# Kernel tuning notes

Measured on AMD Instinct MI355X. Metric: run time of the kernel, lower is better.

The kernel has to match this reference:

```python
import jax, jax.numpy as jnp
import numpy as np

B, C, N = 8, 512, 2048
C8 = C // 8


def setup_inputs() -> dict:
    key = jax.random.key(0)
    kx, kq, kk, kv, kg = jax.random.split(key, 5)
    return {
        "x": jax.random.normal(kx, (B, C, N), dtype=jnp.float32),
        "Wq": jax.random.normal(kq, (C8, C), dtype=jnp.float32) * (1.0 / np.sqrt(C)),
        "Wk": jax.random.normal(kk, (C8, C), dtype=jnp.float32) * (1.0 / np.sqrt(C)),
        "Wv": jax.random.normal(kv, (C, C), dtype=jnp.float32) * (1.0 / np.sqrt(C)),
        # torch init is gamma=0.0; use a small random value so the attention
        # branch contributes to the output.
        "gamma": jax.random.uniform(kg, (1,), dtype=jnp.float32),
    }


def reference(x, Wq, Wk, Wv, gamma):
    # 1x1 convs == per-position linear maps over channels
    f = jnp.einsum("oc,bcn->bon", Wq, x)   # [B, C/8, N]
    g = jnp.einsum("oc,bcn->bon", Wk, x)   # [B, C/8, N]
    h = jnp.einsum("oc,bcn->bon", Wv, x)   # [B, C,   N]
    # scores[b,n,m] = sum_c f[b,c,n] * g[b,c,m]  (unscaled, as in source)
    scores = jnp.einsum("bcn,bcm->bnm", f, g)  # [B, N, N]
    # softmax over dim=1 (the query-position axis) — atypical but faithful
    beta = jax.nn.softmax(scores, axis=1)
    # o = gamma * h @ beta + x
    o = gamma[0] * jnp.einsum("bcn,bnm->bcm", h, beta) + x
    return o
```

## Files before the change

kernel.cpp:

```cpp
#include <hip/hip_runtime.h>
#include <hip/hip_bf16.h>
#include <math.h>

#define NB 8
#define NC 512
#define NN 2048

typedef unsigned short u16;
typedef __attribute__((ext_vector_type(8))) short short8;
typedef __attribute__((ext_vector_type(4))) float f32x4;

__device__ __forceinline__ float bf16_to_f32(u16 v) {
  union { unsigned int u; float f; } c; c.u = ((unsigned int)v) << 16; return c.f;
}
__device__ __forceinline__ u16 f32_to_bf16(float f) {
  __hip_bfloat16 h = __float2bfloat16(f);
  union { __hip_bfloat16 h; u16 u; } c; c.h = h; return c.u;
}
__device__ __forceinline__ void split2(float v, unsigned short& hi, unsigned short& lo) {
  hi = f32_to_bf16(v);
  lo = f32_to_bf16(v - bf16_to_f32(hi));
}

__device__ __forceinline__ void stage128x32(const u16* __restrict__ src, size_t row_base,
                                            int selems, int k0, u16* lds, int tid) {
#pragma unroll
  for (int s = 0; s < 2; ++s) {
    int flat = s * 4096 + tid * 16;
    int row = flat >> 6;
    int kb  = flat & 63;
    const char* g = (const char*)(src + (row_base + row) * (size_t)selems + k0) + kb;
    u16* l = lds + s * 2048 + (tid & ~63) * 8;
    __builtin_amdgcn_global_load_lds(
        (const __attribute__((address_space(1))) unsigned int*)g,
        (__attribute__((address_space(3))) unsigned int*)l, 16, 0, 0);
  }
}

__device__ __forceinline__ void stage128x64_sw(const u16* __restrict__ src, size_t row_base,
                                               int selems, int k0, u16* lds, int tid) {
#pragma unroll
  for (int s = 0; s < 4; ++s) {
    int flat = s * 4096 + tid * 16;
    int row   = flat >> 7;
    int chunk = (flat >> 4) & 7;
    int kb    = (chunk ^ (row & 7)) << 4;
    const char* g = (const char*)(src + (row_base + row) * (size_t)selems + k0) + kb;
    u16* l = lds + s * 2048 + (tid & ~63) * 8;
    __builtin_amdgcn_global_load_lds(
        (const __attribute__((address_space(1))) unsigned int*)g,
        (__attribute__((address_space(3))) unsigned int*)l, 16, 0, 0);
  }
}

__global__ __launch_bounds__(256)
void wsplit_kernel(const float* __restrict__ Wq, const float* __restrict__ Wk,
                   const float* __restrict__ Wv, u16* __restrict__ Whi,
                   u16* __restrict__ Wlo) {
  int idx = (blockIdx.x * 256 + threadIdx.x) * 4;
  int r = idx >> 9, c = idx & 511;
  const float* src;
  if (r < 64)       src = Wq + (size_t)r * NC + c;
  else if (r < 128) src = Wk + (size_t)(r - 64) * NC + c;
  else              src = Wv + (size_t)(r - 128) * NC + c;
  float4 v = *(const float4*)src;
  ushort4 hi, lo;
  split2(v.x, hi.x, lo.x); split2(v.y, hi.y, lo.y);
  split2(v.z, hi.z, lo.z); split2(v.w, hi.w, lo.w);
  *(ushort4*)&Whi[idx] = hi;
  *(ushort4*)&Wlo[idx] = lo;
}

__global__ __launch_bounds__(256)
void xsplit_kernel(const float* __restrict__ x, u16* __restrict__ xThi,
                   u16* __restrict__ xTlo) {
  const int b = blockIdx.z, c0 = blockIdx.y * 64, n0 = blockIdx.x * 64;
  __shared__ float t[64][65];
  const int tid = threadIdx.x, tx = tid & 15, ty = tid >> 4;
#pragma unroll
  for (int r = 0; r < 4; ++r) {
    int c = r * 16 + ty;
    float4 v = *(const float4*)&x[((size_t)b * NC + c0 + c) * NN + n0 + tx * 4];
    t[c][tx * 4 + 0] = v.x; t[c][tx * 4 + 1] = v.y;
    t[c][tx * 4 + 2] = v.z; t[c][tx * 4 + 3] = v.w;
  }
  __syncthreads();
#pragma unroll
  for (int r = 0; r < 4; ++r) {
    int n = r * 16 + ty;
    ushort4 hi, lo;
    split2(t[tx * 4 + 0][n], hi.x, lo.x);
    split2(t[tx * 4 + 1][n], hi.y, lo.y);
    split2(t[tx * 4 + 2][n], hi.z, lo.z);
    split2(t[tx * 4 + 3][n], hi.w, lo.w);
    size_t off = ((size_t)b * NN + n0 + n) * NC + c0 + tx * 4;
    *(ushort4*)&xThi[off] = hi;
    *(ushort4*)&xTlo[off] = lo;
  }
}

__global__ __launch_bounds__(256)
void proj_mfma_kernel(const u16* __restrict__ xThi, const u16* __restrict__ xTlo,
                      const u16* __restrict__ Whi, const u16* __restrict__ Wlo,
                      u16* __restrict__ fgThi, u16* __restrict__ fgTlo,
                      u16* __restrict__ hw) {
  const int b  = blockIdx.z;
  const int n0 = blockIdx.x * 128;
  const int r0 = blockIdx.y * 128;
  const bool fg = (r0 == 0);

  __shared__ u16 Wh[128 * 32], Wl[128 * 32], Xh[128 * 32], Xl[128 * 32];

  const int tid = threadIdx.x, wave = tid >> 6, lane = tid & 63;
  const int quad = lane >> 4, l16 = lane & 15;
  const int wa = (wave >> 1) * 64, wb = (wave & 1) * 64;
  const size_t xrow = (size_t)b * NN + n0;

  f32x4 acc[4][4];
#pragma unroll
  for (int i = 0; i < 4; ++i)
#pragma unroll
    for (int j = 0; j < 4; ++j) acc[i][j] = (f32x4){0.f, 0.f, 0.f, 0.f};

  for (int k0 = 0; k0 < NC; k0 += 32) {
    __syncthreads();
    stage128x32(Whi, r0, NC, k0, Wh, tid);
    stage128x32(xThi, xrow, NC, k0, Xh, tid);
    if (fg) {
      stage128x32(Wlo, r0, NC, k0, Wl, tid);
      stage128x32(xTlo, xrow, NC, k0, Xl, tid);
    }
    __syncthreads();

    if (fg) {
      short8 ah[4], al[4], bh[4], bl[4];
#pragma unroll
      for (int i = 0; i < 4; ++i) {
        ah[i] = *(short8*)&Wh[(wa + i * 16 + l16) * 32 + quad * 8];
        al[i] = *(short8*)&Wl[(wa + i * 16 + l16) * 32 + quad * 8];
      }
#pragma unroll
      for (int j = 0; j < 4; ++j) {
        bh[j] = *(short8*)&Xh[(wb + j * 16 + l16) * 32 + quad * 8];
        bl[j] = *(short8*)&Xl[(wb + j * 16 + l16) * 32 + quad * 8];
      }
#pragma unroll
      for (int i = 0; i < 4; ++i)
#pragma unroll
        for (int j = 0; j < 4; ++j) {
          acc[i][j] = __builtin_amdgcn_mfma_f32_16x16x32_bf16(ah[i], bh[j], acc[i][j], 0, 0, 0);
          acc[i][j] = __builtin_amdgcn_mfma_f32_16x16x32_bf16(ah[i], bl[j], acc[i][j], 0, 0, 0);
          acc[i][j] = __builtin_amdgcn_mfma_f32_16x16x32_bf16(al[i], bh[j], acc[i][j], 0, 0, 0);
        }
    } else {
      short8 ah[4], bh[4];
#pragma unroll
      for (int i = 0; i < 4; ++i)
        ah[i] = *(short8*)&Xh[(wa + i * 16 + l16) * 32 + quad * 8];
#pragma unroll
      for (int j = 0; j < 4; ++j)
        bh[j] = *(short8*)&Wh[(wb + j * 16 + l16) * 32 + quad * 8];
#pragma unroll
      for (int i = 0; i < 4; ++i)
#pragma unroll
        for (int j = 0; j < 4; ++j)
          acc[i][j] = __builtin_amdgcn_mfma_f32_16x16x32_bf16(ah[i], bh[j], acc[i][j], 0, 0, 0);
    }
  }

  if (fg) {
#pragma unroll
    for (int i = 0; i < 4; ++i)
#pragma unroll
      for (int j = 0; j < 4; ++j) {
        int rb = wa + i * 16 + quad * 4;
        int n  = n0 + wb + j * 16 + l16;
        ushort4 hi, lo;
        split2(acc[i][j][0], hi.x, lo.x); split2(acc[i][j][1], hi.y, lo.y);
        split2(acc[i][j][2], hi.z, lo.z); split2(acc[i][j][3], hi.w, lo.w);
        size_t off = ((size_t)b * NN + n) * 128 + rb;
        *(ushort4*)&fgThi[off] = hi;
        *(ushort4*)&fgTlo[off] = lo;
      }
  } else {
#pragma unroll
    for (int i = 0; i < 4; ++i)
#pragma unroll
      for (int j = 0; j < 4; ++j) {
        int nb = n0 + wa + i * 16 + quad * 4;
        int c  = r0 - 128 + wb + j * 16 + l16;
        ushort4 hi;
        hi.x = f32_to_bf16(acc[i][j][0]); hi.y = f32_to_bf16(acc[i][j][1]);
        hi.z = f32_to_bf16(acc[i][j][2]); hi.w = f32_to_bf16(acc[i][j][3]);
        *(ushort4*)&hw[((size_t)b * NC + c) * NN + nb] = hi;
      }
  }
}

__global__ __launch_bounds__(256)
void score_exp_kernel(const u16* __restrict__ fgThi, const u16* __restrict__ fgTlo,
                      u16* __restrict__ E, float* __restrict__ denom) {
  const int b = blockIdx.z;
  const int n0 = blockIdx.x * 128;
  const int m0 = blockIdx.y * 128;

  __shared__ u16 Fh[2][128 * 32], Fl[2][128 * 32], Gh[2][128 * 32], Gl[2][128 * 32];

  const int tid = threadIdx.x, wave = tid >> 6, lane = tid & 63;
  const int quad = lane >> 4, l16 = lane & 15;
  const int wn = (wave >> 1) * 64, wm = (wave & 1) * 64;

  const size_t nrow = (size_t)b * NN + n0;
  const size_t mrow = (size_t)b * NN + m0;
  stage128x32(fgThi, nrow, 128, 0,  Fh[0], tid);
  stage128x32(fgThi, nrow, 128, 32, Fh[1], tid);
  stage128x32(fgTlo, nrow, 128, 0,  Fl[0], tid);
  stage128x32(fgTlo, nrow, 128, 32, Fl[1], tid);
  stage128x32(fgThi, mrow, 128, 64, Gh[0], tid);
  stage128x32(fgThi, mrow, 128, 96, Gh[1], tid);
  stage128x32(fgTlo, mrow, 128, 64, Gl[0], tid);
  stage128x32(fgTlo, mrow, 128, 96, Gl[1], tid);
  __syncthreads();

  f32x4 acc[4][4];
#pragma unroll
  for (int i = 0; i < 4; ++i)
#pragma unroll
    for (int j = 0; j < 4; ++j) acc[i][j] = (f32x4){0.f, 0.f, 0.f, 0.f};

#pragma unroll
  for (int ks = 0; ks < 2; ++ks) {
    short8 ah[4], al[4], bh[4], bl[4];
#pragma unroll
    for (int i = 0; i < 4; ++i) {
      ah[i] = *(short8*)&Fh[ks][(wn + i * 16 + l16) * 32 + quad * 8];
      al[i] = *(short8*)&Fl[ks][(wn + i * 16 + l16) * 32 + quad * 8];
    }
#pragma unroll
    for (int j = 0; j < 4; ++j) {
      bh[j] = *(short8*)&Gh[ks][(wm + j * 16 + l16) * 32 + quad * 8];
      bl[j] = *(short8*)&Gl[ks][(wm + j * 16 + l16) * 32 + quad * 8];
    }
#pragma unroll
    for (int i = 0; i < 4; ++i)
#pragma unroll
      for (int j = 0; j < 4; ++j) {
        acc[i][j] = __builtin_amdgcn_mfma_f32_16x16x32_bf16(ah[i], bh[j], acc[i][j], 0, 0, 0);
        acc[i][j] = __builtin_amdgcn_mfma_f32_16x16x32_bf16(ah[i], bl[j], acc[i][j], 0, 0, 0);
        acc[i][j] = __builtin_amdgcn_mfma_f32_16x16x32_bf16(al[i], bh[j], acc[i][j], 0, 0, 0);
      }
  }

  const size_t brow = (size_t)b * NN;
#pragma unroll
  for (int j = 0; j < 4; ++j) {
    const int m = m0 + wm + j * 16 + l16;
    float psum = 0.f;
#pragma unroll
    for (int i = 0; i < 4; ++i) {
      float e0 = __expf(acc[i][j][0]);
      float e1 = __expf(acc[i][j][1]);
      float e2 = __expf(acc[i][j][2]);
      float e3 = __expf(acc[i][j][3]);
      psum += (e0 + e1) + (e2 + e3);
      ushort4 pk;
      pk.x = f32_to_bf16(e0); pk.y = f32_to_bf16(e1);
      pk.z = f32_to_bf16(e2); pk.w = f32_to_bf16(e3);
      *(ushort4*)&E[(brow + m) * NN + n0 + wn + i * 16 + quad * 4] = pk;
    }
    psum += __shfl_xor(psum, 16);
    psum += __shfl_xor(psum, 32);
    if (quad == 0) atomicAdd(&denom[brow + m], psum);
  }
}

__global__ __launch_bounds__(256)
void out_mfma_kernel(const u16* __restrict__ hw, const u16* __restrict__ E,
                     const float* __restrict__ denom, const float* __restrict__ x,
                     const float* __restrict__ gamma, float* __restrict__ out) {
  const int s = blockIdx.x;
  const int xcd = s & 7;
  const int t = s >> 3;
  const int ct = t & 3;
  const int q = t >> 2;
  const int p = (q << 3) | xcd;
  const int b = p >> 4;
  const int mt = p & 15;
  const int c0 = ct * 128;
  const int m0 = mt * 128;

  __shared__ u16 As[2][128 * 64];
  __shared__ u16 Bs[2][128 * 64];

  const int tid  = threadIdx.x;
  const int wave = tid >> 6;
  const int lane = tid & 63;
  const int quad = lane >> 4;
  const int l16  = lane & 15;
  const int wc = (wave >> 1) * 64;
  const int wm = (wave & 1) * 64;

  f32x4 acc[4][4];
#pragma unroll
  for (int i = 0; i < 4; ++i)
#pragma unroll
    for (int j = 0; j < 4; ++j) acc[i][j] = (f32x4){0.f, 0.f, 0.f, 0.f};

  const size_t hrow = (size_t)b * NC + c0;
  const size_t brow = (size_t)b * NN + m0;

  stage128x64_sw(hw, hrow, NN, 0, As[0], tid);
  stage128x64_sw(E,  brow, NN, 0, Bs[0], tid);

  const int KIT = NN / 64;
  for (int it = 0; it < KIT; ++it) {
    const int cur = it & 1;
    __syncthreads();
    if (it + 1 < KIT) {
      stage128x64_sw(hw, hrow, NN, (it + 1) * 64, As[cur ^ 1], tid);
      stage128x64_sw(E,  brow, NN, (it + 1) * 64, Bs[cur ^ 1], tid);
    }

#pragma unroll
    for (int ks = 0; ks < 2; ++ks) {
      short8 ah[4], bf[4];
#pragma unroll
      for (int i = 0; i < 4; ++i) {
        int rr = wc + i * 16 + l16;
        int ch = ks * 4 + quad;
        ah[i] = *(short8*)&As[cur][rr * 64 + ((ch ^ (rr & 7)) << 3)];
      }
#pragma unroll
      for (int j = 0; j < 4; ++j) {
        int rr = wm + j * 16 + l16;
        int ch = ks * 4 + quad;
        bf[j] = *(short8*)&Bs[cur][rr * 64 + ((ch ^ (rr & 7)) << 3)];
      }

#pragma unroll
      for (int i = 0; i < 4; ++i)
#pragma unroll
        for (int j = 0; j < 4; ++j)
          acc[i][j] = __builtin_amdgcn_mfma_f32_16x16x32_bf16(ah[i], bf[j], acc[i][j], 0, 0, 0);
    }
  }

  const float g = gamma[0];
  float invd[4];
#pragma unroll
  for (int j = 0; j < 4; ++j)
    invd[j] = g / denom[(size_t)b * NN + m0 + wm + j * 16 + l16];

#pragma unroll
  for (int i = 0; i < 4; ++i) {
#pragma unroll
    for (int j = 0; j < 4; ++j) {
      const int c = c0 + wc + i * 16 + quad * 4;
      const int m = m0 + wm + j * 16 + l16;
#pragma unroll
      for (int r = 0; r < 4; ++r) {
        size_t off = ((size_t)b * NC + c + r) * NN + m;
        out[off] = fmaf(invd[j], acc[i][j][r], x[off]);
      }
    }
  }
}

extern "C" void kernel_launch(void* const* d_in, const int* in_sizes, int n_in,
                              void* d_out, int out_size, void* d_ws, size_t ws_size,
                              hipStream_t stream) {
  const float* x     = (const float*)d_in[0];
  const float* Wq    = (const float*)d_in[1];
  const float* Wk    = (const float*)d_in[2];
  const float* Wv    = (const float*)d_in[3];
  const float* gamma = (const float*)d_in[4];
  float* out = (float*)d_out;

  char* ws = (char*)d_ws;
  u16*   E     = (u16*)ws;
  u16*   xThi  = (u16*)ws;
  u16*   xTlo  = (u16*)(ws + 16777216);
  u16*   Whi   = (u16*)(ws + 33554432);
  u16*   Wlo   = (u16*)(ws + 34209792);
  u16*   fgThi = (u16*)(ws + 67108864);
  u16*   fgTlo = (u16*)(ws + 71303168);
  u16*   hw    = (u16*)(ws + 75497472);
  float* denom = (float*)(ws + 109051904);

  wsplit_kernel<<<dim3(320), 256, 0, stream>>>(Wq, Wk, Wv, Whi, Wlo);
  xsplit_kernel<<<dim3(NN / 64, NC / 64, NB), 256, 0, stream>>>(x, xThi, xTlo);
  proj_mfma_kernel<<<dim3(NN / 128, 5, NB), 256, 0, stream>>>(
      xThi, xTlo, Whi, Wlo, fgThi, fgTlo, hw);
  hipMemsetAsync(denom, 0, NB * NN * sizeof(float), stream);
  score_exp_kernel<<<dim3(NN / 128, NN / 128, NB), 256, 0, stream>>>(fgThi, fgTlo, E, denom);
  out_mfma_kernel<<<dim3(512), 256, 0, stream>>>(hw, E, denom, x, gamma, out);
}
```

Measured before the change: 227.3 us.

## Deepen out-kernel pipeline to 4-stage K=32 buffers and fold denom zeroing

The output GEMM now uses four K=32 LDS buffers instead of two K=64 buffers. It prefetches three stages ahead and waits with explicit vmcnt counters rather than a full barrier drain, so global loads overlap MFMA work more deeply. The LDS swizzle is adapted to the 32-wide rows. The separate hipMemsetAsync for denom is replaced by zeroing inside wsplit_kernel, which removes one launch. The risks are that the hand-written vmcnt counts may not match the actual instruction count, and that the loop now runs twice as many iterations with a barrier in each.

Result: slower. 235.4 us (+3.6%).

```diff
diff --git a/kernel.cpp b/kernel.cpp
--- a/kernel.cpp
+++ b/kernel.cpp
@@ -37,14 +37,14 @@
   }
 }
 
-__device__ __forceinline__ void stage128x64_sw(const u16* __restrict__ src, size_t row_base,
+__device__ __forceinline__ void stage128x32_sw(const u16* __restrict__ src, size_t row_base,
                                                int selems, int k0, u16* lds, int tid) {
 #pragma unroll
-  for (int s = 0; s < 4; ++s) {
+  for (int s = 0; s < 2; ++s) {
     int flat = s * 4096 + tid * 16;
-    int row   = flat >> 7;
-    int chunk = (flat >> 4) & 7;
-    int kb    = (chunk ^ (row & 7)) << 4;
+    int row  = flat >> 6;
+    int p    = (flat >> 4) & 3;
+    int kb   = (p ^ ((row >> 1) & 3)) << 4;
     const char* g = (const char*)(src + (row_base + row) * (size_t)selems + k0) + kb;
     u16* l = lds + s * 2048 + (tid & ~63) * 8;
     __builtin_amdgcn_global_load_lds(
@@ -56,8 +56,10 @@
 __global__ __launch_bounds__(256)
 void wsplit_kernel(const float* __restrict__ Wq, const float* __restrict__ Wk,
                    const float* __restrict__ Wv, u16* __restrict__ Whi,
-                   u16* __restrict__ Wlo) {
-  int idx = (blockIdx.x * 256 + threadIdx.x) * 4;
+                   u16* __restrict__ Wlo, float* __restrict__ denom) {
+  int flat = blockIdx.x * 256 + threadIdx.x;
+  if (flat < NB * NN) denom[flat] = 0.f;
+  int idx = flat * 4;
   int r = idx >> 9, c = idx & 511;
   const float* src;
   if (r < 64)       src = Wq + (size_t)r * NC + c;
@@ -289,8 +291,8 @@
   const int c0 = ct * 128;
   const int m0 = mt * 128;
 
-  __shared__ u16 As[2][128 * 64];
-  __shared__ u16 Bs[2][128 * 64];
+  __shared__ u16 As[4][128 * 32];
+  __shared__ u16 Bs[4][128 * 32];
 
   const int tid  = threadIdx.x;
   const int wave = tid >> 6;
@@ -309,40 +311,44 @@
   const size_t hrow = (size_t)b * NC + c0;
   const size_t brow = (size_t)b * NN + m0;
 
-  stage128x64_sw(hw, hrow, NN, 0, As[0], tid);
-  stage128x64_sw(E,  brow, NN, 0, Bs[0], tid);
-
-  const int KIT = NN / 64;
+  stage128x32_sw(hw, hrow, NN, 0,  As[0], tid);
+  stage128x32_sw(E,  brow, NN, 0,  Bs[0], tid);
+  stage128x32_sw(hw, hrow, NN, 32, As[1], tid);
+  stage128x32_sw(E,  brow, NN, 32, Bs[1], tid);
+  stage128x32_sw(hw, hrow, NN, 64, As[2], tid);
+  stage128x32_sw(E,  brow, NN, 64, Bs[2], tid);
+
+  const int KIT = NN / 32;
   for (int it = 0; it < KIT; ++it) {
-    const int cur = it & 1;
-    __syncthreads();
-    if (it + 1 < KIT) {
-      stage128x64_sw(hw, hrow, NN, (it + 1) * 64, As[cur ^ 1], tid);
-      stage128x64_sw(E,  brow, NN, (it + 1) * 64, Bs[cur ^ 1], tid);
-    }
-
-#pragma unroll
-    for (int ks = 0; ks < 2; ++ks) {
-      short8 ah[4], bf[4];
-#pragma unroll
-      for (int i = 0; i < 4; ++i) {
-        int rr = wc + i * 16 + l16;
-        int ch = ks * 4 + quad;
-        ah[i] = *(short8*)&As[cur][rr * 64 + ((ch ^ (rr & 7)) << 3)];
-      }
-#pragma unroll
-      for (int j = 0; j < 4; ++j) {
-        int rr = wm + j * 16 + l16;
-        int ch = ks * 4 + quad;
-        bf[j] = *(short8*)&Bs[cur][rr * 64 + ((ch ^ (rr & 7)) << 3)];
-      }
-
-#pragma unroll
-      for (int i = 0; i < 4; ++i)
-#pragma unroll
-        for (int j = 0; j < 4; ++j)
-          acc[i][j] = __builtin_amdgcn_mfma_f32_16x16x32_bf16(ah[i], bf[j], acc[i][j], 0, 0, 0);
-    }
+    if (it < KIT - 2)       asm volatile("s_waitcnt vmcnt(8)" ::: "memory");
+    else if (it == KIT - 2) asm volatile("s_waitcnt vmcnt(4)" ::: "memory");
+    else                    asm volatile("s_waitcnt vmcnt(0)" ::: "memory");
+    __builtin_amdgcn_s_barrier();
+    asm volatile("" ::: "memory");
+
+    if (it + 3 < KIT) {
+      const int nb = (it + 3) & 3;
+      stage128x32_sw(hw, hrow, NN, (it + 3) * 32, As[nb], tid);
+      stage128x32_sw(E,  brow, NN, (it + 3) * 32, Bs[nb], tid);
+    }
+
+    const int cur = it & 3;
+    short8 ah[4], bf[4];
+#pragma unroll
+    for (int i = 0; i < 4; ++i) {
+      int rr = wc + i * 16 + l16;
+      ah[i] = *(short8*)&As[cur][rr * 32 + ((quad ^ ((rr >> 1) & 3)) << 3)];
+    }
+#pragma unroll
+    for (int j = 0; j < 4; ++j) {
+      int rr = wm + j * 16 + l16;
+      bf[j] = *(short8*)&Bs[cur][rr * 32 + ((quad ^ ((rr >> 1) & 3)) << 3)];
+    }
+#pragma unroll
+    for (int i = 0; i < 4; ++i)
+#pragma unroll
+      for (int j = 0; j < 4; ++j)
+        acc[i][j] = __builtin_amdgcn_mfma_f32_16x16x32_bf16(ah[i], bf[j], acc[i][j], 0, 0, 0);
   }
 
   const float g = gamma[0];
@@ -387,11 +393,10 @@
   u16*   hw    = (u16*)(ws + 75497472);
   float* denom = (float*)(ws + 109051904);
 
-  wsplit_kernel<<<dim3(320), 256, 0, stream>>>(Wq, Wk, Wv, Whi, Wlo);
+  wsplit_kernel<<<dim3(320), 256, 0, stream>>>(Wq, Wk, Wv, Whi, Wlo, denom);
   xsplit_kernel<<<dim3(NN / 64, NC / 64, NB), 256, 0, stream>>>(x, xThi, xTlo);
   proj_mfma_kernel<<<dim3(NN / 128, 5, NB), 256, 0, stream>>>(
       xThi, xTlo, Whi, Wlo, fgThi, fgTlo, hw);
-  hipMemsetAsync(denom, 0, NB * NN * sizeof(float), stream);
   score_exp_kernel<<<dim3(NN / 128, NN / 128, NB), 256, 0, stream>>>(fgThi, fgTlo, E, denom);
   out_mfma_kernel<<<dim3(512), 256, 0, stream>>>(hw, E, denom, x, gamma, out);
 }
```

## Fuse score/exp and output GEMM into a flash-style attention kernel

Applied to the files above, without the earlier changes.

Replaces the separate score-exp kernel, which wrote a full bf16 exp matrix E to global memory, and the out GEMM kernel that read it back, with a single fused kernel. Each 512-thread block holds a 128-column m tile and 256 channels, recomputes its scores per 64-row n chunk, puts exp values in LDS, and accumulates h@P immediately. Column sums are reduced in-block, which removes the global denom memset and atomics. The cost is that scores are computed twice, once per channel half, and the grid shrinks to 256 blocks with more per-block work and LDS use.

Measured after the change: 207.5 us. -8.7%, faster.

```diff
diff --git a/kernel.cpp b/kernel.cpp
--- a/kernel.cpp
+++ b/kernel.cpp
@@ -20,6 +20,12 @@
 __device__ __forceinline__ void split2(float v, unsigned short& hi, unsigned short& lo) {
   hi = f32_to_bf16(v);
   lo = f32_to_bf16(v - bf16_to_f32(hi));
+}
+
+__device__ __forceinline__ void gl_lds16(const void* g, void* l) {
+  __builtin_amdgcn_global_load_lds(
+      (const __attribute__((address_space(1))) unsigned int*)g,
+      (__attribute__((address_space(3))) unsigned int*)l, 16, 0, 0);
 }
 
 __device__ __forceinline__ void stage128x32(const u16* __restrict__ src, size_t row_base,
@@ -31,25 +37,7 @@
     int kb  = flat & 63;
     const char* g = (const char*)(src + (row_base + row) * (size_t)selems + k0) + kb;
     u16* l = lds + s * 2048 + (tid & ~63) * 8;
-    __builtin_amdgcn_global_load_lds(
-        (const __attribute__((address_space(1))) unsigned int*)g,
-        (__attribute__((address_space(3))) unsigned int*)l, 16, 0, 0);
-  }
-}
-
-__device__ __forceinline__ void stage128x64_sw(const u16* __restrict__ src, size_t row_base,
-                                               int selems, int k0, u16* lds, int tid) {
-#pragma unroll
-  for (int s = 0; s < 4; ++s) {
-    int flat = s * 4096 + tid * 16;
-    int row   = flat >> 7;
-    int chunk = (flat >> 4) & 7;
-    int kb    = (chunk ^ (row & 7)) << 4;
-    const char* g = (const char*)(src + (row_base + row) * (size_t)selems + k0) + kb;
-    u16* l = lds + s * 2048 + (tid & ~63) * 8;
-    __builtin_amdgcn_global_load_lds(
-        (const __attribute__((address_space(1))) unsigned int*)g,
-        (__attribute__((address_space(3))) unsigned int*)l, 16, 0, 0);
+    gl_lds16(g, l);
   }
 }
 
@@ -197,170 +185,185 @@
   }
 }
 
-__global__ __launch_bounds__(256)
-void score_exp_kernel(const u16* __restrict__ fgThi, const u16* __restrict__ fgTlo,
-                      u16* __restrict__ E, float* __restrict__ denom) {
-  const int b = blockIdx.z;
-  const int n0 = blockIdx.x * 128;
-  const int m0 = blockIdx.y * 128;
-
-  __shared__ u16 Fh[2][128 * 32], Fl[2][128 * 32], Gh[2][128 * 32], Gl[2][128 * 32];
-
-  const int tid = threadIdx.x, wave = tid >> 6, lane = tid & 63;
-  const int quad = lane >> 4, l16 = lane & 15;
-  const int wn = (wave >> 1) * 64, wm = (wave & 1) * 64;
-
-  const size_t nrow = (size_t)b * NN + n0;
-  const size_t mrow = (size_t)b * NN + m0;
-  stage128x32(fgThi, nrow, 128, 0,  Fh[0], tid);
-  stage128x32(fgThi, nrow, 128, 32, Fh[1], tid);
-  stage128x32(fgTlo, nrow, 128, 0,  Fl[0], tid);
-  stage128x32(fgTlo, nrow, 128, 32, Fl[1], tid);
-  stage128x32(fgThi, mrow, 128, 64, Gh[0], tid);
-  stage128x32(fgThi, mrow, 128, 96, Gh[1], tid);
-  stage128x32(fgTlo, mrow, 128, 64, Gl[0], tid);
-  stage128x32(fgTlo, mrow, 128, 96, Gl[1], tid);
-  __syncthreads();
-
-  f32x4 acc[4][4];
-#pragma unroll
-  for (int i = 0; i < 4; ++i)
-#pragma unroll
-    for (int j = 0; j < 4; ++j) acc[i][j] = (f32x4){0.f, 0.f, 0.f, 0.f};
-
-#pragma unroll
-  for (int ks = 0; ks < 2; ++ks) {
-    short8 ah[4], al[4], bh[4], bl[4];
-#pragma unroll
-    for (int i = 0; i < 4; ++i) {
-      ah[i] = *(short8*)&Fh[ks][(wn + i * 16 + l16) * 32 + quad * 8];
-      al[i] = *(short8*)&Fl[ks][(wn + i * 16 + l16) * 32 + quad * 8];
-    }
-#pragma unroll
-    for (int j = 0; j < 4; ++j) {
-      bh[j] = *(short8*)&Gh[ks][(wm + j * 16 + l16) * 32 + quad * 8];
-      bl[j] = *(short8*)&Gl[ks][(wm + j * 16 + l16) * 32 + quad * 8];
-    }
-#pragma unroll
-    for (int i = 0; i < 4; ++i)
-#pragma unroll
-      for (int j = 0; j < 4; ++j) {
-        acc[i][j] = __builtin_amdgcn_mfma_f32_16x16x32_bf16(ah[i], bh[j], acc[i][j], 0, 0, 0);
-        acc[i][j] = __builtin_amdgcn_mfma_f32_16x16x32_bf16(ah[i], bl[j], acc[i][j], 0, 0, 0);
-        acc[i][j] = __builtin_amdgcn_mfma_f32_16x16x32_bf16(al[i], bh[j], acc[i][j], 0, 0, 0);
-      }
-  }
-
-  const size_t brow = (size_t)b * NN;
-#pragma unroll
-  for (int j = 0; j < 4; ++j) {
-    const int m = m0 + wm + j * 16 + l16;
-    float psum = 0.f;
-#pragma unroll
-    for (int i = 0; i < 4; ++i) {
-      float e0 = __expf(acc[i][j][0]);
-      float e1 = __expf(acc[i][j][1]);
-      float e2 = __expf(acc[i][j][2]);
-      float e3 = __expf(acc[i][j][3]);
-      psum += (e0 + e1) + (e2 + e3);
-      ushort4 pk;
-      pk.x = f32_to_bf16(e0); pk.y = f32_to_bf16(e1);
-      pk.z = f32_to_bf16(e2); pk.w = f32_to_bf16(e3);
-      *(ushort4*)&E[(brow + m) * NN + n0 + wn + i * 16 + quad * 4] = pk;
-    }
-    psum += __shfl_xor(psum, 16);
-    psum += __shfl_xor(psum, 32);
-    if (quad == 0) atomicAdd(&denom[brow + m], psum);
-  }
-}
-
-__global__ __launch_bounds__(256)
-void out_mfma_kernel(const u16* __restrict__ hw, const u16* __restrict__ E,
-                     const float* __restrict__ denom, const float* __restrict__ x,
+__global__ __launch_bounds__(512)
+void attn_out_kernel(const u16* __restrict__ fgThi, const u16* __restrict__ fgTlo,
+                     const u16* __restrict__ hw, const float* __restrict__ x,
                      const float* __restrict__ gamma, float* __restrict__ out) {
   const int s = blockIdx.x;
   const int xcd = s & 7;
   const int t = s >> 3;
-  const int ct = t & 3;
-  const int q = t >> 2;
-  const int p = (q << 3) | xcd;
-  const int b = p >> 4;
-  const int mt = p & 15;
-  const int c0 = ct * 128;
+  const int mt = t & 15;
+  const int hi5 = t >> 4;
+  const int p = (hi5 << 3) | xcd;
+  const int b = p >> 1;
+  const int ch = p & 1;
   const int m0 = mt * 128;
-
-  __shared__ u16 As[2][128 * 64];
-  __shared__ u16 Bs[2][128 * 64];
-
-  const int tid  = threadIdx.x;
-  const int wave = tid >> 6;
-  const int lane = tid & 63;
-  const int quad = lane >> 4;
-  const int l16  = lane & 15;
-  const int wc = (wave >> 1) * 64;
-  const int wm = (wave & 1) * 64;
-
-  f32x4 acc[4][4];
+  const int c0 = ch * 256;
+
+  __shared__ u16 Fh[2][64 * 64], Fl[2][64 * 64];
+  __shared__ u16 Hs[2][256 * 64];
+  __shared__ u16 Ps[128 * 64];
+  __shared__ float Dn[128];
+
+  const int tid = threadIdx.x, wave = tid >> 6, lane = tid & 63;
+  const int quad = lane >> 4, l16 = lane & 15;
+  const int ws_n = (wave >> 2) * 32, ws_m = (wave & 3) * 32;
+  const int wv_c = (wave >> 1) * 64, wv_m = (wave & 1) * 64;
+
+  const size_t frow = (size_t)b * NN;
+  const size_t hrow = (size_t)b * NC + c0;
+
+  short8 gh[2][2], gl[2][2];
+#pragma unroll
+  for (int j = 0; j < 2; ++j)
+#pragma unroll
+    for (int k = 0; k < 2; ++k) {
+      size_t o = (frow + m0 + ws_m + j * 16 + l16) * 128 + 64 + k * 32 + quad * 8;
+      gh[j][k] = *(const short8*)&fgThi[o];
+      gl[j][k] = *(const short8*)&fgTlo[o];
+    }
+
+  {
+    int flat = tid * 16;
+    int row = flat >> 7, chunk = (flat >> 4) & 7;
+    int kb = ((chunk ^ (row & 7)) << 4);
+    gl_lds16((const char*)(fgThi + (frow + row) * 128) + kb, Fh[0] + (tid & ~63) * 8);
+    gl_lds16((const char*)(fgTlo + (frow + row) * 128) + kb, Fl[0] + (tid & ~63) * 8);
+#pragma unroll
+    for (int s2 = 0; s2 < 4; ++s2) {
+      int f2 = s2 * 8192 + tid * 16;
+      int r2 = f2 >> 7, c2 = (f2 >> 4) & 7;
+      gl_lds16((const char*)(hw + (hrow + r2) * NN) + ((c2 ^ (r2 & 7)) << 4),
+               Hs[0] + s2 * 4096 + (tid & ~63) * 8);
+    }
+  }
+  __syncthreads();
+
+  float dsum0 = 0.f, dsum1 = 0.f;
+  f32x4 ao[4][4];
 #pragma unroll
   for (int i = 0; i < 4; ++i)
 #pragma unroll
-    for (int j = 0; j < 4; ++j) acc[i][j] = (f32x4){0.f, 0.f, 0.f, 0.f};
-
-  const size_t hrow = (size_t)b * NC + c0;
-  const size_t brow = (size_t)b * NN + m0;
-
-  stage128x64_sw(hw, hrow, NN, 0, As[0], tid);
-  stage128x64_sw(E,  brow, NN, 0, Bs[0], tid);
-
-  const int KIT = NN / 64;
-  for (int it = 0; it < KIT; ++it) {
+    for (int j = 0; j < 4; ++j) ao[i][j] = (f32x4){0.f, 0.f, 0.f, 0.f};
+
+  for (int it = 0; it < NN / 64; ++it) {
     const int cur = it & 1;
+    if (it + 1 < NN / 64) {
+      const int n1 = (it + 1) * 64;
+      int flat = tid * 16;
+      int row = flat >> 7, chunk = (flat >> 4) & 7;
+      int kb = ((chunk ^ (row & 7)) << 4);
+      gl_lds16((const char*)(fgThi + (frow + n1 + row) * 128) + kb,
+               Fh[cur ^ 1] + (tid & ~63) * 8);
+      gl_lds16((const char*)(fgTlo + (frow + n1 + row) * 128) + kb,
+               Fl[cur ^ 1] + (tid & ~63) * 8);
+#pragma unroll
+      for (int s2 = 0; s2 < 4; ++s2) {
+        int f2 = s2 * 8192 + tid * 16;
+        int r2 = f2 >> 7, c2 = (f2 >> 4) & 7;
+        gl_lds16((const char*)(hw + (hrow + r2) * NN + n1) + ((c2 ^ (r2 & 7)) << 4),
+                 Hs[cur ^ 1] + s2 * 4096 + (tid & ~63) * 8);
+      }
+    }
+
+    f32x4 as[2][2];
+#pragma unroll
+    for (int i = 0; i < 2; ++i)
+#pragma unroll
+      for (int j = 0; j < 2; ++j) as[i][j] = (f32x4){0.f, 0.f, 0.f, 0.f};
+#pragma unroll
+    for (int k = 0; k < 2; ++k) {
+      short8 fh[2], fl[2];
+#pragma unroll
+      for (int i = 0; i < 2; ++i) {
+        int rr = ws_n + i * 16 + l16;
+        int ci = (((k * 4 + quad) ^ (rr & 7)) << 3);
+        fh[i] = *(short8*)&Fh[cur][rr * 64 + ci];
+        fl[i] = *(short8*)&Fl[cur][rr * 64 + ci];
+      }
+#pragma unroll
+      for (int i = 0; i < 2; ++i)
+#pragma unroll
+        for (int j = 0; j < 2; ++j) {
+          as[i][j] = __builtin_amdgcn_mfma_f32_16x16x32_bf16(fh[i], gh[j][k], as[i][j], 0, 0, 0);
+          as[i][j] = __builtin_amdgcn_mfma_f32_16x16x32_bf16(fh[i], gl[j][k], as[i][j], 0, 0, 0);
+          as[i][j] = __builtin_amdgcn_mfma_f32_16x16x32_bf16(fl[i], gh[j][k], as[i][j], 0, 0, 0);
+        }
+    }
+
+#pragma unroll
+    for (int j = 0; j < 2; ++j) {
+      int m = ws_m + j * 16 + l16;
+#pragma unroll
+      for (int i = 0; i < 2; ++i) {
+        float e0 = __expf(as[i][j][0]);
+        float e1 = __expf(as[i][j][1]);
+        float e2 = __expf(as[i][j][2]);
+        float e3 = __expf(as[i][j][3]);
+        if (j == 0) dsum0 += (e0 + e1) + (e2 + e3);
+        else        dsum1 += (e0 + e1) + (e2 + e3);
+        ushort4 pk;
+        pk.x = f32_to_bf16(e0); pk.y = f32_to_bf16(e1);
+        pk.z = f32_to_bf16(e2); pk.w = f32_to_bf16(e3);
+        int nb = ws_n * 2 + i * 32 + quad * 8;
+        int chunk = nb >> 4;
+        int off = (nb & 15) >> 1;
+        *(ushort4*)&Ps[m * 64 + ((chunk ^ (m & 7)) << 3) + off] = pk;
+      }
+    }
+
+    asm volatile("s_waitcnt lgkmcnt(0)" ::: "memory");
+    __builtin_amdgcn_s_barrier();
+
+#pragma unroll
+    for (int k = 0; k < 2; ++k) {
+      short8 hh[4], pb[4];
+#pragma unroll
+      for (int i = 0; i < 4; ++i) {
+        int rr = wv_c + i * 16 + l16;
+        hh[i] = *(short8*)&Hs[cur][rr * 64 + ((((k * 4 + quad)) ^ (rr & 7)) << 3)];
+      }
+#pragma unroll
+      for (int j = 0; j < 4; ++j) {
+        int rm = wv_m + j * 16 + l16;
+        pb[j] = *(short8*)&Ps[rm * 64 + ((((k * 4 + quad)) ^ (rm & 7)) << 3)];
+      }
+#pragma unroll
+      for (int i = 0; i < 4; ++i)
+#pragma unroll
+        for (int j = 0; j < 4; ++j)
+          ao[i][j] = __builtin_amdgcn_mfma_f32_16x16x32_bf16(hh[i], pb[j], ao[i][j], 0, 0, 0);
+    }
+
     __syncthreads();
-    if (it + 1 < KIT) {
-      stage128x64_sw(hw, hrow, NN, (it + 1) * 64, As[cur ^ 1], tid);
-      stage128x64_sw(E,  brow, NN, (it + 1) * 64, Bs[cur ^ 1], tid);
-    }
-
-#pragma unroll
-    for (int ks = 0; ks < 2; ++ks) {
-      short8 ah[4], bf[4];
-#pragma unroll
-      for (int i = 0; i < 4; ++i) {
-        int rr = wc + i * 16 + l16;
-        int ch = ks * 4 + quad;
-        ah[i] = *(short8*)&As[cur][rr * 64 + ((ch ^ (rr & 7)) << 3)];
-      }
-#pragma unroll
-      for (int j = 0; j < 4; ++j) {
-        int rr = wm + j * 16 + l16;
-        int ch = ks * 4 + quad;
-        bf[j] = *(short8*)&Bs[cur][rr * 64 + ((ch ^ (rr & 7)) << 3)];
-      }
-
-#pragma unroll
-      for (int i = 0; i < 4; ++i)
-#pragma unroll
-        for (int j = 0; j < 4; ++j)
-          acc[i][j] = __builtin_amdgcn_mfma_f32_16x16x32_bf16(ah[i], bf[j], acc[i][j], 0, 0, 0);
-    }
-  }
+  }
+
+  dsum0 += __shfl_xor(dsum0, 16); dsum0 += __shfl_xor(dsum0, 32);
+  dsum1 += __shfl_xor(dsum1, 16); dsum1 += __shfl_xor(dsum1, 32);
+  if (tid < 128) Dn[tid] = 0.f;
+  __syncthreads();
+  if (quad == 0) {
+    atomicAdd(&Dn[ws_m + l16], dsum0);
+    atomicAdd(&Dn[ws_m + 16 + l16], dsum1);
+  }
+  __syncthreads();
 
   const float g = gamma[0];
   float invd[4];
 #pragma unroll
   for (int j = 0; j < 4; ++j)
-    invd[j] = g / denom[(size_t)b * NN + m0 + wm + j * 16 + l16];
+    invd[j] = g / Dn[wv_m + j * 16 + l16];
 
 #pragma unroll
   for (int i = 0; i < 4; ++i) {
 #pragma unroll
     for (int j = 0; j < 4; ++j) {
-      const int c = c0 + wc + i * 16 + quad * 4;
-      const int m = m0 + wm + j * 16 + l16;
+      const int c = c0 + wv_c + i * 16 + quad * 4;
+      const int m = m0 + wv_m + j * 16 + l16;
 #pragma unroll
       for (int r = 0; r < 4; ++r) {
         size_t off = ((size_t)b * NC + c + r) * NN + m;
-        out[off] = fmaf(invd[j], acc[i][j][r], x[off]);
+        out[off] = fmaf(invd[j], ao[i][j][r], x[off]);
       }
     }
   }
@@ -377,7 +380,6 @@
   float* out = (float*)d_out;
 
   char* ws = (char*)d_ws;
-  u16*   E     = (u16*)ws;
   u16*   xThi  = (u16*)ws;
   u16*   xTlo  = (u16*)(ws + 16777216);
   u16*   Whi   = (u16*)(ws + 33554432);
@@ -385,13 +387,10 @@
   u16*   fgThi = (u16*)(ws + 67108864);
   u16*   fgTlo = (u16*)(ws + 71303168);
   u16*   hw    = (u16*)(ws + 75497472);
-  float* denom = (float*)(ws + 109051904);
 
   wsplit_kernel<<<dim3(320), 256, 0, stream>>>(Wq, Wk, Wv, Whi, Wlo);
   xsplit_kernel<<<dim3(NN / 64, NC / 64, NB), 256, 0, stream>>>(x, xThi, xTlo);
   proj_mfma_kernel<<<dim3(NN / 128, 5, NB), 256, 0, stream>>>(
       xThi, xTlo, Whi, Wlo, fgThi, fgTlo, hw);
-  hipMemsetAsync(denom, 0, NB * NN * sizeof(float), stream);
-  score_exp_kernel<<<dim3(NN / 128, NN / 128, NB), 256, 0, stream>>>(fgThi, fgTlo, E, denom);
-  out_mfma_kernel<<<dim3(512), 256, 0, stream>>>(hw, E, denom, x, gamma, out);
-}
+  attn_out_kernel<<<dim3(256), 512, 0, stream>>>(fgThi, fgTlo, hw, x, gamma, out);
+}
```
